# Kernel optimization log

Measured on AMD Instinct MI355X. Metric: run time of the kernel, lower is better.

## Reference

```python
import jax, jax.numpy as jnp
import numpy as np

IN_F, OUT_F = 4096, 11008
B, S = 2, 4096


def setup_inputs() -> dict:
    key = jax.random.key(0)
    k1, k2, k3, k4 = jax.random.split(key, 4)
    x = jax.random.normal(k1, (B, S, IN_F), dtype=jnp.float32) * 3.0  # pre-smoothed activations
    # int8 weight, stored as int8 (spec'd int32 for harness; math identical)
    weight = jax.random.randint(k2, (OUT_F, IN_F), -127, 128, dtype=jnp.int32).astype(jnp.int8)
    bias = jax.random.normal(k3, (OUT_F,), dtype=jnp.float32)
    dequant_scale = jax.random.uniform(k4, (1,), dtype=jnp.float32) * 0.01 + 0.001  # weight absmax scale
    return {"x": x, "weight": weight, "bias": bias, "dequant_scale": dequant_scale}


def reference(x, weight, bias, dequant_scale):
    x_shape = x.shape
    x2 = x.reshape(-1, x_shape[-1])  # [T, in]
    # per-token activation quantization: absmax -> scale -> round/clamp to int8
    quant_scale = (jnp.max(jnp.abs(x2), axis=-1, keepdims=True) / 127.0).astype(jnp.float32)  # [T,1]
    x_q = jnp.clip(jnp.round(x2 / quant_scale), -128, 127).astype(jnp.int8)
    out_i32 = jnp.matmul(x_q.astype(jnp.int32), weight.astype(jnp.int32).T)  # [T, out]
    # dequant epilogue + bias (all fp32)
    dscale = dequant_scale.reshape(()) * quant_scale  # [T,1]
    out = dscale * out_i32.astype(jnp.float32) + bias
    return out.reshape(*x_shape[:-1], -1).astype(x.dtype)
```

## Files before the change

kernel.cpp:

```cpp
#include <hip/hip_runtime.h>

#define T_TOKENS 8192
#define IN_F 4096
#define OUT_F 11008

#define BM 256
#define BN 256
#define NT (IN_F / 64)

typedef __attribute__((ext_vector_type(4))) int v4i;
typedef __attribute__((ext_vector_type(16))) int v16i;

__device__ __forceinline__ void load_lds16(const signed char* g, const signed char* l) {
    __builtin_amdgcn_global_load_lds(
        (const __attribute__((address_space(1))) void*)g,
        (__attribute__((address_space(3))) void*)l, 16, 0, 0);
}


__global__ __launch_bounds__(256) void quant_repack_kernel(
        const float* __restrict__ x, signed char* __restrict__ xq,
        float* __restrict__ qscale, const int* __restrict__ w32,
        signed char* __restrict__ w8) {
    if (blockIdx.x < T_TOKENS) {
        const int row = blockIdx.x;
        const int t = threadIdx.x;
        const float4* xr = (const float4*)(x + (size_t)row * IN_F) + t * 4;
        float4 v[4];
        float am = 0.f;
#pragma unroll
        for (int i = 0; i < 4; ++i) {
            v[i] = xr[i];
            am = fmaxf(am, fmaxf(fmaxf(fabsf(v[i].x), fabsf(v[i].y)),
                                 fmaxf(fabsf(v[i].z), fabsf(v[i].w))));
        }
#pragma unroll
        for (int off = 32; off > 0; off >>= 1)
            am = fmaxf(am, __shfl_xor(am, off, 64));
        __shared__ float wmax[4];
        const int wv = t >> 6;
        if ((t & 63) == 0) wmax[wv] = am;
        __syncthreads();
        float amax = fmaxf(fmaxf(wmax[0], wmax[1]), fmaxf(wmax[2], wmax[3]));
        float qs = amax * (1.0f / 127.0f);
        if (qs < 1e-30f) qs = 1e-30f;
        const float inv = 1.0f / qs;
        if (t == 0) qscale[row] = qs;
        int q[16];
#pragma unroll
        for (int i = 0; i < 4; ++i) {
            q[i * 4 + 0] = max(-128, min(127, (int)rintf(v[i].x * inv)));
            q[i * 4 + 1] = max(-128, min(127, (int)rintf(v[i].y * inv)));
            q[i * 4 + 2] = max(-128, min(127, (int)rintf(v[i].z * inv)));
            q[i * 4 + 3] = max(-128, min(127, (int)rintf(v[i].w * inv)));
        }
        v4i p;
#pragma unroll
        for (int i = 0; i < 4; ++i)
            p[i] = (q[i * 4] & 255) | ((q[i * 4 + 1] & 255) << 8) |
                   ((q[i * 4 + 2] & 255) << 16) | ((q[i * 4 + 3] & 255) << 24);
        const int k32 = t >> 1, hi = t & 1;
        *(v4i*)(xq + (((size_t)(row >> 5)) * 128 + k32) * 1024 +
                ((hi * 32) + (row & 31)) * 16) = p;
    } else {
        const int bb = blockIdx.x - T_TOKENS;
        const int nblk = bb >> 5;
        const int kg = bb & 31;
        const int t = threadIdx.x;
        __shared__ signed char tile[32][144];
        const int rrow = t >> 3, c8 = t & 7;
        const int* src = w32 + (size_t)(nblk * 32 + rrow) * IN_F + kg * 128 + c8 * 16;
        v4i pk;
#pragma unroll
        for (int j = 0; j < 4; ++j) {
            v4i w = ((const v4i*)src)[j];
            pk[j] = (w[0] & 255) | ((w[1] & 255) << 8) |
                    ((w[2] & 255) << 16) | ((w[3] & 255) << 24);
        }
        *(v4i*)&tile[rrow][c8 * 16] = pk;
        __syncthreads();
        const int k32l = t >> 6, lane = t & 63;
        const int hi = lane >> 5, l31 = lane & 31;
        v4i o = *(const v4i*)&tile[l31][k32l * 32 + hi * 16];
        *(v4i*)(w8 + ((size_t)(nblk)*128 + kg * 4 + k32l) * 1024 + lane * 16) = o;
    }
}

__global__ __launch_bounds__(512, 2) void gemm_kernel(
        const signed char* __restrict__ A, const signed char* __restrict__ B,
        const float* __restrict__ qscale, const float* __restrict__ bias,
        const float* __restrict__ dqs, float* __restrict__ out) {
    __shared__ __align__(16) signed char smem[4 * 16384];

    const int tid = threadIdx.x;
    const int wid = tid >> 6;
    const int lane = tid & 63;
    const int wm = wid >> 2;
    const int wn = wid & 3;
    const int l31 = lane & 31;
    const int hi = lane >> 5;

    const int b = (int)blockIdx.x;
    const int xcd = b & 7;
    const int idx = b >> 3;
    const int m0 = (xcd * 4 + (idx & 3)) * BM;
    const int n0 = (idx >> 2) * BN;

    const signed char* aSrc[2];
    int ldsA[2];
#pragma unroll
    for (int c = 0; c < 2; ++c) {
        const int mloc = c * 4 + (wid >> 1);
        const int inner = (wid & 1) * 1024 + lane * 16;
        aSrc[c] = A + ((size_t)((m0 >> 5) + mloc)) * 131072 + inner;
        ldsA[c] = c * 8192 + wid * 1024;
    }
    const signed char* bSrc[2];
#pragma unroll
    for (int in = 0; in < 2; ++in)
        bSrc[in] = B + ((size_t)((n0 >> 5) + wn * 2 + in)) * 131072 + lane * 16;

    v16i acc[4][2] = {};
    v4i Bf0[4], Bf1[4], Bf2[4], Bf3[4];

#pragma unroll
    for (int tt = 0; tt < 3; ++tt) {
        load_lds16(aSrc[0] + tt * 2048, smem + tt * 16384 + ldsA[0]);
        load_lds16(aSrc[1] + tt * 2048, smem + tt * 16384 + ldsA[1]);
    }
    __builtin_amdgcn_sched_barrier(0);
#pragma unroll
    for (int in = 0; in < 2; ++in)
#pragma unroll
        for (int ks = 0; ks < 2; ++ks) {
            Bf0[in * 2 + ks] = *(const v4i*)(bSrc[in] + ks * 1024);
            Bf1[in * 2 + ks] = *(const v4i*)(bSrc[in] + 2048 + ks * 1024);
        }

#define SUB(tau, j, Bcur, Bld) do {                                            \
    if ((tau) == 0)                                                            \
        asm volatile("s_waitcnt vmcnt(12)" ::: "memory");                      \
    else if ((tau) + 3 < NT)                                                   \
        asm volatile("s_waitcnt vmcnt(16)" ::: "memory");                      \
    else                                                                       \
        asm volatile("s_waitcnt vmcnt(8)" ::: "memory");                       \
    __builtin_amdgcn_sched_barrier(0);                                         \
    __builtin_amdgcn_s_barrier();                                              \
    __builtin_amdgcn_sched_barrier(0);                                         \
    if ((tau) + 3 < NT) {                                                      \
        load_lds16(aSrc[0] + ((tau) + 3) * 2048,                               \
                   smem + (((j) + 3) & 3) * 16384 + ldsA[0]);                  \
        load_lds16(aSrc[1] + ((tau) + 3) * 2048,                               \
                   smem + (((j) + 3) & 3) * 16384 + ldsA[1]);                  \
    }                                                                          \
    __builtin_amdgcn_sched_barrier(0);                                         \
    if ((tau) + 2 < NT) {                                                      \
        _Pragma("unroll")                                                      \
        for (int in = 0; in < 2; ++in)                                         \
            _Pragma("unroll")                                                  \
            for (int ks = 0; ks < 2; ++ks)                                     \
                Bld[in * 2 + ks] = *(const v4i*)(bSrc[in] +                    \
                    ((size_t)((tau) + 2)) * 2048 + ks * 1024);                 \
    }                                                                          \
    v4i afr[4][2];                                                             \
    _Pragma("unroll")                                                          \
    for (int im = 0; im < 4; ++im)                                             \
        _Pragma("unroll")                                                      \
        for (int ks = 0; ks < 2; ++ks)                                         \
            afr[im][ks] = *(const v4i*)(smem + (j) * 16384 +                   \
                (wm * 4 + im) * 2048 + ks * 1024 + lane * 16);                 \
    __builtin_amdgcn_s_setprio(1);                                             \
    _Pragma("unroll")                                                          \
    for (int ks = 0; ks < 2; ++ks)                                             \
        _Pragma("unroll")                                                      \
        for (int im = 0; im < 4; ++im)                                         \
            _Pragma("unroll")                                                  \
            for (int in = 0; in < 2; ++in)                                     \
                acc[im][in] = __builtin_amdgcn_mfma_i32_32x32x32_i8(           \
                    afr[im][ks], Bcur[in * 2 + ks], acc[im][in], 0, 0, 0);     \
    __builtin_amdgcn_s_setprio(0);                                             \
} while (0)

    for (int tt = 0; tt < NT; tt += 4) {
        SUB(tt + 0, 0, Bf0, Bf2);
        SUB(tt + 1, 1, Bf1, Bf3);
        SUB(tt + 2, 2, Bf2, Bf0);
        SUB(tt + 3, 3, Bf3, Bf1);
    }
#undef SUB

    const float dq = dqs[0];
#pragma unroll
    for (int im = 0; im < 4; ++im) {
        float qsv[16];
#pragma unroll
        for (int r = 0; r < 16; ++r) {
            const int trow = wm * 128 + im * 32 + (r & 3) + 8 * (r >> 2) + 4 * hi;
            qsv[r] = dq * qscale[m0 + trow];
        }
#pragma unroll
        for (int in = 0; in < 2; ++in) {
            const int col = n0 + wn * 64 + in * 32 + l31;
            const float bv = bias[col];
#pragma unroll
            for (int r = 0; r < 16; ++r) {
                const int trow = wm * 128 + im * 32 + (r & 3) + 8 * (r >> 2) + 4 * hi;
                out[(size_t)(m0 + trow) * OUT_F + col] =
                    qsv[r] * (float)acc[im][in][r] + bv;
            }
        }
    }
}

extern "C" void kernel_launch(void* const* d_in, const int* in_sizes, int n_in,
                              void* d_out, int out_size, void* d_ws, size_t ws_size,
                              hipStream_t stream) {
    const float* x    = (const float*)d_in[0];
    const int*   w32  = (const int*)d_in[1];
    const float* bias = (const float*)d_in[2];
    const float* dqs  = (const float*)d_in[3];
    float* out = (float*)d_out;

    signed char* xq = (signed char*)d_ws;
    float* qscale   = (float*)((char*)d_ws + (size_t)T_TOKENS * IN_F);
    signed char* w8 = (signed char*)((char*)d_ws + (size_t)T_TOKENS * IN_F
                                     + (size_t)T_TOKENS * 4);

    quant_repack_kernel<<<T_TOKENS + (OUT_F / 32) * 32, 256, 0, stream>>>(
        x, xq, qscale, w32, w8);
    dim3 g((T_TOKENS / BM) * (OUT_F / BN));
    gemm_kernel<<<g, 512, 0, stream>>>(xq, w8, qscale, bias, dqs, out);
}
```

Before: 556.7 us.

## Stage B operand through LDS with a five-deep async global-to-LDS ring

The weight (B) tile now also goes through LDS with global_load_lds, instead of each wave loading its own fragments from global memory into registers. This removes the duplicate B loads shared across wave rows and frees registers. The A/B pipeline becomes a 5-buffer ring of 32 KB stages with vmcnt-based waits, followed by a 4-phase drain. The ring uses 160 KB of LDS per block, which likely allows only one block per CU despite launch bounds asking for two, trading occupancy for deeper prefetch.

```diff
diff --git a/kernel.cpp b/kernel.cpp
--- a/kernel.cpp
+++ b/kernel.cpp
@@ -90,7 +90,8 @@
         const signed char* __restrict__ A, const signed char* __restrict__ B,
         const float* __restrict__ qscale, const float* __restrict__ bias,
         const float* __restrict__ dqs, float* __restrict__ out) {
-    __shared__ __align__(16) signed char smem[4 * 16384];
+    __shared__ __align__(16) signed char smem_[5 * 32768];
+    signed char* smem = smem_;
 
     const int tid = threadIdx.x;
     const int wid = tid >> 6;
@@ -106,88 +107,90 @@
     const int m0 = (xcd * 4 + (idx & 3)) * BM;
     const int n0 = (idx >> 2) * BN;
 
-    const signed char* aSrc[2];
-    int ldsA[2];
+    const signed char* aS[2];
+    const signed char* bS[2];
+    int ldsA[2], ldsB[2];
 #pragma unroll
     for (int c = 0; c < 2; ++c) {
-        const int mloc = c * 4 + (wid >> 1);
-        const int inner = (wid & 1) * 1024 + lane * 16;
-        aSrc[c] = A + ((size_t)((m0 >> 5) + mloc)) * 131072 + inner;
-        ldsA[c] = c * 8192 + wid * 1024;
-    }
-    const signed char* bSrc[2];
+        aS[c] = A + ((size_t)((m0 >> 5) + wid)) * 131072 + c * 1024 + lane * 16;
+        bS[c] = B + ((size_t)((n0 >> 5) + wid)) * 131072 + c * 1024 + lane * 16;
+        ldsA[c] = wid * 2048 + c * 1024;
+        ldsB[c] = 16384 + wid * 2048 + c * 1024;
+    }
+    int rdA[4][2], rdB[2][2];
+#pragma unroll
+    for (int im = 0; im < 4; ++im)
+#pragma unroll
+        for (int ks = 0; ks < 2; ++ks)
+            rdA[im][ks] = (wm * 4 + im) * 2048 + ks * 1024 + lane * 16;
 #pragma unroll
     for (int in = 0; in < 2; ++in)
-        bSrc[in] = B + ((size_t)((n0 >> 5) + wn * 2 + in)) * 131072 + lane * 16;
+#pragma unroll
+        for (int ks = 0; ks < 2; ++ks)
+            rdB[in][ks] = 16384 + (wn * 2 + in) * 2048 + ks * 1024 + lane * 16;
 
     v16i acc[4][2] = {};
-    v4i Bf0[4], Bf1[4], Bf2[4], Bf3[4];
-
-#pragma unroll
-    for (int tt = 0; tt < 3; ++tt) {
-        load_lds16(aSrc[0] + tt * 2048, smem + tt * 16384 + ldsA[0]);
-        load_lds16(aSrc[1] + tt * 2048, smem + tt * 16384 + ldsA[1]);
-    }
-    __builtin_amdgcn_sched_barrier(0);
-#pragma unroll
-    for (int in = 0; in < 2; ++in)
-#pragma unroll
-        for (int ks = 0; ks < 2; ++ks) {
-            Bf0[in * 2 + ks] = *(const v4i*)(bSrc[in] + ks * 1024);
-            Bf1[in * 2 + ks] = *(const v4i*)(bSrc[in] + 2048 + ks * 1024);
-        }
-
-#define SUB(tau, j, Bcur, Bld) do {                                            \
-    if ((tau) == 0)                                                            \
-        asm volatile("s_waitcnt vmcnt(12)" ::: "memory");                      \
-    else if ((tau) + 3 < NT)                                                   \
-        asm volatile("s_waitcnt vmcnt(16)" ::: "memory");                      \
-    else                                                                       \
-        asm volatile("s_waitcnt vmcnt(8)" ::: "memory");                       \
+
+#pragma unroll
+    for (int tt = 0; tt < 4; ++tt)
+#pragma unroll
+        for (int c = 0; c < 2; ++c) {
+            load_lds16(aS[c] + tt * 2048, smem + tt * 32768 + ldsA[c]);
+            load_lds16(bS[c] + tt * 2048, smem + tt * 32768 + ldsB[c]);
+        }
+
+#define PH(BUF, SBUF, KT, VMC, DOSTAGE) do {                                   \
+    asm volatile("s_waitcnt vmcnt(" #VMC ") lgkmcnt(0)" ::: "memory");         \
     __builtin_amdgcn_sched_barrier(0);                                         \
     __builtin_amdgcn_s_barrier();                                              \
     __builtin_amdgcn_sched_barrier(0);                                         \
-    if ((tau) + 3 < NT) {                                                      \
-        load_lds16(aSrc[0] + ((tau) + 3) * 2048,                               \
-                   smem + (((j) + 3) & 3) * 16384 + ldsA[0]);                  \
-        load_lds16(aSrc[1] + ((tau) + 3) * 2048,                               \
-                   smem + (((j) + 3) & 3) * 16384 + ldsA[1]);                  \
+    if (DOSTAGE) {                                                             \
+        const int ko_ = (KT) * 2048;                                           \
+        _Pragma("unroll")                                                      \
+        for (int c = 0; c < 2; ++c) {                                          \
+            load_lds16(aS[c] + ko_, smem + (SBUF) * 32768 + ldsA[c]);          \
+            load_lds16(bS[c] + ko_, smem + (SBUF) * 32768 + ldsB[c]);          \
+        }                                                                      \
     }                                                                          \
     __builtin_amdgcn_sched_barrier(0);                                         \
-    if ((tau) + 2 < NT) {                                                      \
+    {                                                                          \
+        const signed char* rb_ = smem + (BUF) * 32768;                         \
+        v4i a_[4][2], bf_[2][2];                                               \
+        _Pragma("unroll")                                                      \
+        for (int im = 0; im < 4; ++im)                                         \
+            _Pragma("unroll")                                                  \
+            for (int ks = 0; ks < 2; ++ks)                                     \
+                a_[im][ks] = *(const v4i*)(rb_ + rdA[im][ks]);                 \
         _Pragma("unroll")                                                      \
         for (int in = 0; in < 2; ++in)                                         \
             _Pragma("unroll")                                                  \
             for (int ks = 0; ks < 2; ++ks)                                     \
-                Bld[in * 2 + ks] = *(const v4i*)(bSrc[in] +                    \
-                    ((size_t)((tau) + 2)) * 2048 + ks * 1024);                 \
+                bf_[in][ks] = *(const v4i*)(rb_ + rdB[in][ks]);                \
+        __builtin_amdgcn_s_setprio(1);                                         \
+        _Pragma("unroll")                                                      \
+        for (int ks = 0; ks < 2; ++ks)                                         \
+            _Pragma("unroll")                                                  \
+            for (int im = 0; im < 4; ++im)                                     \
+                _Pragma("unroll")                                              \
+                for (int in = 0; in < 2; ++in)                                 \
+                    acc[im][in] = __builtin_amdgcn_mfma_i32_32x32x32_i8(       \
+                        a_[im][ks], bf_[in][ks], acc[im][in], 0, 0, 0);        \
+        __builtin_amdgcn_s_setprio(0);                                         \
     }                                                                          \
-    v4i afr[4][2];                                                             \
-    _Pragma("unroll")                                                          \
-    for (int im = 0; im < 4; ++im)                                             \
-        _Pragma("unroll")                                                      \
-        for (int ks = 0; ks < 2; ++ks)                                         \
-            afr[im][ks] = *(const v4i*)(smem + (j) * 16384 +                   \
-                (wm * 4 + im) * 2048 + ks * 1024 + lane * 16);                 \
-    __builtin_amdgcn_s_setprio(1);                                             \
-    _Pragma("unroll")                                                          \
-    for (int ks = 0; ks < 2; ++ks)                                             \
-        _Pragma("unroll")                                                      \
-        for (int im = 0; im < 4; ++im)                                         \
-            _Pragma("unroll")                                                  \
-            for (int in = 0; in < 2; ++in)                                     \
-                acc[im][in] = __builtin_amdgcn_mfma_i32_32x32x32_i8(           \
-                    afr[im][ks], Bcur[in * 2 + ks], acc[im][in], 0, 0, 0);     \
-    __builtin_amdgcn_s_setprio(0);                                             \
 } while (0)
 
-    for (int tt = 0; tt < NT; tt += 4) {
-        SUB(tt + 0, 0, Bf0, Bf2);
-        SUB(tt + 1, 1, Bf1, Bf3);
-        SUB(tt + 2, 2, Bf2, Bf0);
-        SUB(tt + 3, 3, Bf3, Bf1);
-    }
-#undef SUB
+    for (int p = 0; p < 60; p += 5) {
+        PH(0, 4, p + 4, 12, 1);
+        PH(1, 0, p + 5, 12, 1);
+        PH(2, 1, p + 6, 12, 1);
+        PH(3, 2, p + 7, 12, 1);
+        PH(4, 3, p + 8, 12, 1);
+    }
+    PH(0, 0, 0, 12, 0);
+    PH(1, 0, 0, 8,  0);
+    PH(2, 0, 0, 4,  0);
+    PH(3, 0, 0, 0,  0);
+#undef PH
 
     const float dq = dqs[0];
 #pragma unroll
```

After: 469.8 us. -15.6%, faster.
